# Kernel optimization log

Measured on AMD Instinct MI355X. Metric: run time of the kernel, lower is better.

The kernel has to match this reference:

```python
import jax, jax.numpy as jnp
import numpy as np

DIM = 1024
D_STATE = 16
D_CONV = 4
EXPAND = 2
D_INNER = EXPAND * DIM
BATCH = 4
SEQ = 2048


def setup_inputs() -> dict:
    key = jax.random.key(0)
    ks = jax.random.split(key, 9)
    n = lambda i, shape, scale=0.02: (jax.random.normal(ks[i], shape, jnp.float32) * scale)
    return {
        "x": jax.random.normal(ks[0], (BATCH, SEQ, DIM), jnp.float32),
        "in_proj_w": n(1, (D_INNER, DIM)),
        "conv_w": n(2, (D_INNER, D_CONV), 0.1),          # depthwise kernel (groups=d_inner)
        "x_proj_w": n(3, (2 * D_STATE + 1, D_INNER)),
        "dt_proj_w": n(4, (D_INNER, 1), 1.0),
        "dt_proj_b": n(5, (D_INNER,), 0.1),
        "A_log": jax.random.normal(ks[6], (D_INNER, D_STATE), jnp.float32),
        "D": jnp.ones((D_INNER,), jnp.float32),
        "out_proj_w": n(7, (DIM, D_INNER)),
        "norm_w": jnp.ones((DIM,), jnp.float32),
        "norm_b": jnp.zeros((DIM,), jnp.float32),
    }


def reference(x, in_proj_w, conv_w, x_proj_w, dt_proj_w, dt_proj_b,
              A_log, D, out_proj_w, norm_w, norm_b):
    Bsz, L, _ = x.shape
    shortcut = x

    # LayerNorm
    mu = jnp.mean(x, axis=-1, keepdims=True)
    var = jnp.var(x, axis=-1, keepdims=True)
    h = (x - mu) / jnp.sqrt(var + 1e-5) * norm_w + norm_b

    # in_proj: [B,L,dim] -> [B,L,d_inner]
    h = h @ in_proj_w.T

    # causal depthwise conv1d (padding d_conv-1, truncate to L)
    hp = jnp.pad(h, ((0, 0), (D_CONV - 1, 0), (0, 0)))
    h_conv = sum(hp[:, k:k + L, :] * conv_w[:, k] for k in range(D_CONV))
    h = jax.nn.silu(h_conv)

    # x_proj -> dt (1), B (d_state), C (d_state)
    proj = h @ x_proj_w.T
    dt_in = proj[..., :1]
    B_param = proj[..., 1:1 + D_STATE]      # [B,L,d_state]
    C_param = proj[..., 1 + D_STATE:]       # [B,L,d_state]
    dt = jax.nn.softplus(dt_in @ dt_proj_w.T + dt_proj_b)  # [B,L,d_inner]

    A = -jnp.exp(A_log)                     # [d_inner, d_state]

    def step(state, inp):
        dt_t, B_t, C_t, x_t = inp           # [B,d_inner],[B,ds],[B,ds],[B,d_inner]
        state = jnp.exp(A[None] * dt_t[:, :, None]) * state \
                + B_t[:, None, :] * x_t[:, :, None]          # [B,d_inner,d_state]
        y = jnp.einsum('bnd,bd->bn', state, C_t) + D * x_t   # [B,d_inner]
        return state, y

    init = jnp.zeros((Bsz, D_INNER, D_STATE), x.dtype)
    xs = (jnp.swapaxes(dt, 0, 1), jnp.swapaxes(B_param, 0, 1),
          jnp.swapaxes(C_param, 0, 1), jnp.swapaxes(h, 0, 1))
    state, ys = jax.lax.scan(step, init, xs)
    y = jnp.swapaxes(ys, 0, 1)              # [B,L,d_inner]

    out = jax.nn.silu(y) @ out_proj_w.T + shortcut
    return out, state
```

## Files before the change

### kernel.cpp

```cpp
#include <hip/hip_runtime.h>

typedef unsigned short u16;
typedef unsigned int u32;
typedef __attribute__((ext_vector_type(8))) short short8;
typedef __attribute__((ext_vector_type(4))) float f32x4;
typedef __attribute__((ext_vector_type(2))) float f32x2;
typedef __attribute__((ext_vector_type(8))) unsigned short ushort8_t;

#define SEQ 2048
#define DIM 1024
#define DINNER 2048
#define NPROJ 33
#define NPROJ_PAD 48
#define LC 32
#define NC 64

__device__ __forceinline__ u16 f2bf(float f) {
  union { float f; u32 u; } v; v.f = f;
  u32 r = (v.u + 0x7fffu + ((v.u >> 16) & 1u)) >> 16;
  return (u16)r;
}
__device__ __forceinline__ float bf2f(u16 s) {
  union { u32 u; float f; } v; v.u = ((u32)s) << 16;
  return v.f;
}
__device__ __forceinline__ float lo_bf(u32 w) {
  union { u32 u; float f; } v; v.u = w << 16; return v.f;
}
__device__ __forceinline__ float hi_bf(u32 w) {
  union { u32 u; float f; } v; v.u = w & 0xffff0000u; return v.f;
}
__device__ __forceinline__ float fexp2(float x) {
#if __has_builtin(__builtin_amdgcn_exp2f)
  return __builtin_amdgcn_exp2f(x);
#else
  return __expf(x * 0.69314718f);
#endif
}
__device__ __forceinline__ float softplus(float x) {
  return fmaxf(x, 0.f) + __logf(1.f + __expf(-fabsf(x)));
}
__device__ __forceinline__ f32x2 sp2(float v) { f32x2 r; r.x = v; r.y = v; return r; }
__device__ __forceinline__ f32x2 pkfma(f32x2 a, f32x2 b, f32x2 c) {
  return __builtin_elementwise_fma(a, b, c);
}
__device__ __forceinline__ void async16(const void* g, void* l) {
  __builtin_amdgcn_global_load_lds(
      (const __attribute__((address_space(1))) u32*)g,
      (__attribute__((address_space(3))) u32*)l, 16, 0, 0);
}

__global__ void cast_w_kernel(const float* __restrict__ w1, const float* __restrict__ w3,
                              u16* __restrict__ o1, u16* __restrict__ o3) {
  int i = blockIdx.x * 256 + threadIdx.x;
  float4 a = ((const float4*)w1)[i];
  float4 b = ((const float4*)w3)[i];
  ushort4 oa, ob;
  oa.x = f2bf(a.x); oa.y = f2bf(a.y); oa.z = f2bf(a.z); oa.w = f2bf(a.w);
  ob.x = f2bf(b.x); ob.y = f2bf(b.y); ob.z = f2bf(b.z); ob.w = f2bf(b.w);
  ((ushort4*)o1)[i] = oa;
  ((ushort4*)o3)[i] = ob;
}

__global__ void cast_w2pad_kernel(const float* __restrict__ src, u16* __restrict__ dst) {
  int i = blockIdx.x * 256 + threadIdx.x;
  int j = i >> 11, k = i & 2047;
  dst[i] = (j < NPROJ) ? f2bf(src[j * 2048 + k]) : (u16)0;
}

__global__ __launch_bounds__(256) void ln_kernel(const float* __restrict__ x,
                                                 const float* __restrict__ w,
                                                 const float* __restrict__ b,
                                                 u16* __restrict__ h) {
  const int row = blockIdx.x;
  const int tid = threadIdx.x;
  const int lane = tid & 63, wave = tid >> 6;
  const float4 v = ((const float4*)(x + (size_t)row * DIM))[tid];
  float s = v.x + v.y + v.z + v.w;
  float q = v.x * v.x + v.y * v.y + v.z * v.z + v.w * v.w;
  for (int off = 32; off; off >>= 1) {
    s += __shfl_down(s, off);
    q += __shfl_down(q, off);
  }
  __shared__ float sbuf[8];
  if (lane == 0) { sbuf[wave] = s; sbuf[4 + wave] = q; }
  __syncthreads();
  float tot = sbuf[0] + sbuf[1] + sbuf[2] + sbuf[3];
  float totq = sbuf[4] + sbuf[5] + sbuf[6] + sbuf[7];
  const float mean = tot * (1.0f / DIM);
  const float var = totq * (1.0f / DIM) - mean * mean;
  const float rs = rsqrtf(var + 1e-5f);
  const float4 wv = ((const float4*)w)[tid];
  const float4 bv = ((const float4*)b)[tid];
  ushort4 o;
  o.x = f2bf((v.x - mean) * rs * wv.x + bv.x);
  o.y = f2bf((v.y - mean) * rs * wv.y + bv.y);
  o.z = f2bf((v.z - mean) * rs * wv.z + bv.z);
  o.w = f2bf((v.w - mean) * rs * wv.w + bv.w);
  ((ushort4*)(h + (size_t)row * DIM))[tid] = o;
}

__global__ __launch_bounds__(512) void gemm_bf16_kernel(const u16* __restrict__ A,
                                                        const u16* __restrict__ Bt,
                                                        u16* __restrict__ C,
                                                        int K, int N) {
  __shared__ u16 As[128 * 32];
  __shared__ u16 Bs[128 * 32];
  const int tid = threadIdx.x;
  const int lane = tid & 63, wave = tid >> 6;
  const int wm = wave >> 2, wn = wave & 3;
  const int row16 = lane & 15, quad = lane >> 4;
  const int flat = blockIdx.x + gridDim.x * blockIdx.y;
  const int xcd = flat & 7;
  const int sidx = flat >> 3;
  const int bm = xcd * 8 + (sidx & 7);
  const int bn = sidx >> 3;
  f32x4 acc[4][2] = {};
  const u16* Ablk = A + (size_t)bm * 128 * K;
  const u16* Bblk = Bt + (size_t)bn * 128 * K;
  const int r = tid >> 2, cc = (tid & 3) * 8;
  for (int k0 = 0; k0 < K; k0 += 32) {
    async16(Ablk + (size_t)r * K + k0 + cc, &As[tid * 8]);
    async16(Bblk + (size_t)r * K + k0 + cc, &Bs[tid * 8]);
    __syncthreads();
    short8 af[4], bfr[2];
#pragma unroll
    for (int i = 0; i < 4; ++i)
      af[i] = *(const short8*)&As[(wm * 64 + i * 16 + row16) * 32 + quad * 8];
#pragma unroll
    for (int j = 0; j < 2; ++j)
      bfr[j] = *(const short8*)&Bs[(wn * 32 + j * 16 + row16) * 32 + quad * 8];
#pragma unroll
    for (int i = 0; i < 4; ++i)
#pragma unroll
      for (int j = 0; j < 2; ++j)
        acc[i][j] = __builtin_amdgcn_mfma_f32_16x16x32_bf16(af[i], bfr[j], acc[i][j], 0, 0, 0);
    __syncthreads();
  }
#pragma unroll
  for (int i = 0; i < 4; ++i) {
    int m = bm * 128 + wm * 64 + i * 16 + quad * 4;
#pragma unroll
    for (int j = 0; j < 2; ++j) {
      int n = bn * 128 + wn * 32 + j * 16 + row16;
#pragma unroll
      for (int rr = 0; rr < 4; ++rr)
        C[(size_t)(m + rr) * N + n] = f2bf(acc[i][j][rr]);
    }
  }
}

__global__ __launch_bounds__(512) void gemm_out_kernel(const u16* __restrict__ A,
                                                       const u16* __restrict__ Bt,
                                                       const float* __restrict__ resid,
                                                       float* __restrict__ C,
                                                       int K, int N) {
  __shared__ u16 As[128 * 32];
  __shared__ u16 Bs[128 * 32];
  const int tid = threadIdx.x;
  const int lane = tid & 63, wave = tid >> 6;
  const int wm = wave >> 2, wn = wave & 3;
  const int row16 = lane & 15, quad = lane >> 4;
  const int flat = blockIdx.x + gridDim.x * blockIdx.y;
  const int xcd = flat & 7;
  const int sidx = flat >> 3;
  const int bm = xcd * 8 + (sidx & 7);
  const int bn = sidx >> 3;
  f32x4 acc[4][2] = {};
  const u16* Ablk = A + (size_t)bm * 128 * K;
  const u16* Bblk = Bt + (size_t)bn * 128 * K;
  const int r = tid >> 2, cc = (tid & 3) * 8;
  for (int k0 = 0; k0 < K; k0 += 32) {
    async16(Ablk + (size_t)r * K + k0 + cc, &As[tid * 8]);
    async16(Bblk + (size_t)r * K + k0 + cc, &Bs[tid * 8]);
    __syncthreads();
    short8 af[4], bfr[2];
#pragma unroll
    for (int i = 0; i < 4; ++i)
      af[i] = *(const short8*)&As[(wm * 64 + i * 16 + row16) * 32 + quad * 8];
#pragma unroll
    for (int j = 0; j < 2; ++j)
      bfr[j] = *(const short8*)&Bs[(wn * 32 + j * 16 + row16) * 32 + quad * 8];
#pragma unroll
    for (int i = 0; i < 4; ++i)
#pragma unroll
      for (int j = 0; j < 2; ++j)
        acc[i][j] = __builtin_amdgcn_mfma_f32_16x16x32_bf16(af[i], bfr[j], acc[i][j], 0, 0, 0);
    __syncthreads();
  }
#pragma unroll
  for (int i = 0; i < 4; ++i) {
    int m = bm * 128 + wm * 64 + i * 16 + quad * 4;
#pragma unroll
    for (int j = 0; j < 2; ++j) {
      int n = bn * 128 + wn * 32 + j * 16 + row16;
#pragma unroll
      for (int rr = 0; rr < 4; ++rr) {
        size_t idx = (size_t)(m + rr) * N + n;
        C[idx] = acc[i][j][rr] + resid[idx];
      }
    }
  }
}

__global__ __launch_bounds__(256) void conv_silu_kernel(const u16* __restrict__ c1,
                                                        const float* __restrict__ cw,
                                                        u16* __restrict__ cs) {
  const int tid = threadIdx.x;
  const int dg = tid * 8;
  const size_t m0 = (size_t)blockIdx.x * 8;
  const int l0 = (int)(m0 & (SEQ - 1));
  float w[4][8];
  {
    const float4* cw4 = (const float4*)(cw + (size_t)dg * 4);
#pragma unroll
    for (int c = 0; c < 8; ++c) {
      float4 v = cw4[c];
      w[0][c] = v.x; w[1][c] = v.y; w[2][c] = v.z; w[3][c] = v.w;
    }
  }
  const u16* base = c1 + m0 * DINNER + dg;
  ushort8_t win0, win1, win2, win3;
  const ushort8_t zero = (ushort8_t)0;
  if (l0 == 0) {
    win0 = zero; win1 = zero; win2 = zero;
  } else {
    win0 = *(const ushort8_t*)(base - 3 * DINNER);
    win1 = *(const ushort8_t*)(base - 2 * DINNER);
    win2 = *(const ushort8_t*)(base - 1 * DINNER);
  }
  win3 = *(const ushort8_t*)(base);
#pragma unroll
  for (int t = 0; t < 8; ++t) {
    ushort8_t nxt = win3;
    if (t < 7) nxt = *(const ushort8_t*)(base + (size_t)(t + 1) * DINNER);
    ushort8_t o;
#pragma unroll
    for (int c = 0; c < 8; ++c) {
      float acc = bf2f((u16)win0[c]) * w[0][c];
      acc = fmaf(bf2f((u16)win1[c]), w[1][c], acc);
      acc = fmaf(bf2f((u16)win2[c]), w[2][c], acc);
      acc = fmaf(bf2f((u16)win3[c]), w[3][c], acc);
      const float s = acc / (1.f + __expf(-acc));
      o[c] = (unsigned short)f2bf(s);
    }
    *(ushort8_t*)(cs + (m0 + t) * DINNER + dg) = o;
    win0 = win1; win1 = win2; win2 = win3; win3 = nxt;
  }
}

__global__ __launch_bounds__(256) void gemm_w2_kernel(const u16* __restrict__ A,
                                                      const u16* __restrict__ Bt,
                                                      float* __restrict__ C) {
  __shared__ u16 As[64 * 32];
  __shared__ u16 Bs[48 * 32];
  const int tid = threadIdx.x;
  const int lane = tid & 63, wave = tid >> 6;
  const int row16 = lane & 15, quad = lane >> 4;
  const int bm = blockIdx.x;
  const int K = DINNER;
  f32x4 acc[3] = {};
  const u16* Ablk = A + (size_t)bm * 64 * K;
  const int r = tid >> 2, cc = (tid & 3) * 8;
  for (int k0 = 0; k0 < K; k0 += 32) {
    async16(Ablk + (size_t)r * K + k0 + cc, &As[tid * 8]);
    if (tid < 192) async16(Bt + (size_t)r * K + k0 + cc, &Bs[tid * 8]);
    __syncthreads();
    short8 af = *(const short8*)&As[(wave * 16 + row16) * 32 + quad * 8];
    short8 bfr[3];
#pragma unroll
    for (int j = 0; j < 3; ++j)
      bfr[j] = *(const short8*)&Bs[(j * 16 + row16) * 32 + quad * 8];
#pragma unroll
    for (int j = 0; j < 3; ++j)
      acc[j] = __builtin_amdgcn_mfma_f32_16x16x32_bf16(af, bfr[j], acc[j], 0, 0, 0);
    __syncthreads();
  }
  const int m = bm * 64 + wave * 16 + quad * 4;
#pragma unroll
  for (int j = 0; j < 3; ++j) {
    const int n = j * 16 + row16;
#pragma unroll
    for (int rr = 0; rr < 4; ++rr)
      C[(size_t)(m + rr) * NPROJ_PAD + n] = acc[j][rr];
  }
}


__global__ __launch_bounds__(128) void scan_phase1(const float* __restrict__ proj,
                                                   const u16* __restrict__ xs,
                                                   const float* __restrict__ dtw_,
                                                   const float* __restrict__ dtb_,
                                                   const float* __restrict__ A_log,
                                                   u16* __restrict__ S,
                                                   float* __restrict__ Tdt) {
  __shared__ float Bsh[LC][16];
  __shared__ float DTin[LC];
  const int tid = threadIdx.x;
  const int d0 = blockIdx.x * 256 + tid * 2;
  const int c = blockIdx.y;
  const int b = blockIdx.z;
  const size_t mrow = (size_t)b * SEQ + c * LC;
  for (int i = tid; i < LC * 16; i += 128) {
    int t = i >> 4, n = i & 15;
    Bsh[t][n] = proj[(mrow + t) * NPROJ_PAD + 1 + n];
  }
  if (tid < LC) DTin[tid] = proj[(mrow + tid) * NPROJ_PAD];
  __syncthreads();
  f32x2 An2[16];
#pragma unroll
  for (int n = 0; n < 16; ++n) {
    An2[n].x = -__expf(A_log[(size_t)d0 * 16 + n]) * 1.44269504f;
    An2[n].y = -__expf(A_log[(size_t)(d0 + 1) * 16 + n]) * 1.44269504f;
  }
  const float2 dtwv = *(const float2*)(dtw_ + d0);
  const float2 dtbv = *(const float2*)(dtb_ + d0);
  f32x2 dtw2; dtw2.x = dtwv.x; dtw2.y = dtwv.y;
  f32x2 dtb2; dtb2.x = dtbv.x; dtb2.y = dtbv.y;
  f32x2 s[16];
#pragma unroll
  for (int n = 0; n < 16; ++n) s[n] = sp2(0.f);
  f32x2 Tsum = sp2(0.f);
  const u16* xp = xs + mrow * DINNER + d0;
  u32 xw = *(const u32*)xp;
#pragma unroll 2
  for (int t = 0; t < LC; ++t) {
    f32x2 xv; xv.x = lo_bf(xw); xv.y = hi_bf(xw);
    if (t + 1 < LC) xw = *(const u32*)(xp + (size_t)(t + 1) * DINNER);
    f32x2 dtv = pkfma(sp2(DTin[t]), dtw2, dtb2);
    f32x2 sp; sp.x = softplus(dtv.x); sp.y = softplus(dtv.y);
    Tsum += sp;
    const float4* Br = (const float4*)&Bsh[t][0];
#pragma unroll
    for (int q = 0; q < 4; ++q) {
      const float4 Bq = Br[q];
      const float bqa[4] = {Bq.x, Bq.y, Bq.z, Bq.w};
#pragma unroll
      for (int j = 0; j < 4; ++j) {
        const int n = q * 4 + j;
        f32x2 e = An2[n] * sp;
        f32x2 dk; dk.x = fexp2(e.x); dk.y = fexp2(e.y);
        s[n] = pkfma(dk, s[n], sp2(bqa[j]) * xv);
      }
    }
  }
  const size_t so = ((size_t)(b * NC + c) * DINNER + d0) * 16;
  ushort8_t o0, o1, o2, o3;
#pragma unroll
  for (int j = 0; j < 8; ++j) {
    o0[j] = f2bf(s[j].x);     o1[j] = f2bf(s[8 + j].x);
    o2[j] = f2bf(s[j].y);     o3[j] = f2bf(s[8 + j].y);
  }
  *(ushort8_t*)(S + so) = o0;       *(ushort8_t*)(S + so + 8) = o1;
  *(ushort8_t*)(S + so + 16) = o2;  *(ushort8_t*)(S + so + 24) = o3;
  *(float2*)(Tdt + (size_t)(b * NC + c) * DINNER + d0) = make_float2(Tsum.x, Tsum.y);
}

__global__ __launch_bounds__(256) void scan_phase2(const float* __restrict__ A_log,
                                                   u16* __restrict__ S,
                                                   const float* __restrict__ Tdt,
                                                   float* __restrict__ out_state) {
  const int idx = blockIdx.x * 256 + threadIdx.x;
  const int nq = idx & 3;
  const int d = (idx >> 2) & (DINNER - 1);
  const int b = idx >> 13;
  float An2[4];
#pragma unroll
  for (int n = 0; n < 4; ++n) An2[n] = -__expf(A_log[d * 16 + nq * 4 + n]) * 1.44269504f;
  float prev[4] = {0.f, 0.f, 0.f, 0.f};
  for (int c = 0; c < NC; ++c) {
    const size_t base = (size_t)(b * NC + c) * DINNER + d;
    const float T = Tdt[base];
    const size_t so = base * 16 + nq * 4;
    ushort4 lv = *(const ushort4*)(S + so);
    const float loc[4] = {bf2f(lv.x), bf2f(lv.y), bf2f(lv.z), bf2f(lv.w)};
    ushort4 pv;
    pv.x = f2bf(prev[0]); pv.y = f2bf(prev[1]); pv.z = f2bf(prev[2]); pv.w = f2bf(prev[3]);
    *(ushort4*)(S + so) = pv;
    const float dk0 = fexp2(An2[0] * T), dk1 = fexp2(An2[1] * T);
    const float dk2 = fexp2(An2[2] * T), dk3 = fexp2(An2[3] * T);
    prev[0] = fmaf(dk0, prev[0], loc[0]);
    prev[1] = fmaf(dk1, prev[1], loc[1]);
    prev[2] = fmaf(dk2, prev[2], loc[2]);
    prev[3] = fmaf(dk3, prev[3], loc[3]);
  }
  *(float4*)(out_state + ((size_t)b * DINNER + d) * 16 + nq * 4) =
      make_float4(prev[0], prev[1], prev[2], prev[3]);
}

__global__ __launch_bounds__(128) void scan_phase3(const float* __restrict__ proj,
                                                   const u16* __restrict__ xs,
                                                   const float* __restrict__ dtw_,
                                                   const float* __restrict__ dtb_,
                                                   const float* __restrict__ A_log,
                                                   const float* __restrict__ Dp,
                                                   const u16* __restrict__ S,
                                                   u16* __restrict__ ysil) {
  __shared__ float Bsh[LC][16];
  __shared__ float Csh[LC][16];
  __shared__ float DTin[LC];
  const int tid = threadIdx.x;
  const int d0 = blockIdx.x * 256 + tid * 2;
  const int c = blockIdx.y;
  const int b = blockIdx.z;
  const size_t mrow = (size_t)b * SEQ + c * LC;
  for (int i = tid; i < LC * 16; i += 128) {
    int t = i >> 4, n = i & 15;
    Bsh[t][n] = proj[(mrow + t) * NPROJ_PAD + 1 + n];
    Csh[t][n] = proj[(mrow + t) * NPROJ_PAD + 17 + n];
  }
  if (tid < LC) DTin[tid] = proj[(mrow + tid) * NPROJ_PAD];
  __syncthreads();
  f32x2 An2[16];
#pragma unroll
  for (int n = 0; n < 16; ++n) {
    An2[n].x = -__expf(A_log[(size_t)d0 * 16 + n]) * 1.44269504f;
    An2[n].y = -__expf(A_log[(size_t)(d0 + 1) * 16 + n]) * 1.44269504f;
  }
  const float2 dtwv = *(const float2*)(dtw_ + d0);
  const float2 dtbv = *(const float2*)(dtb_ + d0);
  const float2 Ddv = *(const float2*)(Dp + d0);
  f32x2 dtw2; dtw2.x = dtwv.x; dtw2.y = dtwv.y;
  f32x2 dtb2; dtb2.x = dtbv.x; dtb2.y = dtbv.y;
  f32x2 Dd2; Dd2.x = Ddv.x; Dd2.y = Ddv.y;
  f32x2 s[16];
  const size_t so = ((size_t)(b * NC + c) * DINNER + d0) * 16;
  {
    ushort8_t v0 = *(const ushort8_t*)(S + so);
    ushort8_t v1 = *(const ushort8_t*)(S + so + 8);
    ushort8_t v2 = *(const ushort8_t*)(S + so + 16);
    ushort8_t v3 = *(const ushort8_t*)(S + so + 24);
#pragma unroll
    for (int j = 0; j < 8; ++j) {
      s[j].x = bf2f((u16)v0[j]);     s[8 + j].x = bf2f((u16)v1[j]);
      s[j].y = bf2f((u16)v2[j]);     s[8 + j].y = bf2f((u16)v3[j]);
    }
  }
  const u16* xp = xs + mrow * DINNER + d0;
  u16* yp = ysil + mrow * DINNER + d0;
  u32 xw = *(const u32*)xp;
#pragma unroll 2
  for (int t = 0; t < LC; ++t) {
    f32x2 xv; xv.x = lo_bf(xw); xv.y = hi_bf(xw);
    if (t + 1 < LC) xw = *(const u32*)(xp + (size_t)(t + 1) * DINNER);
    f32x2 dtv = pkfma(sp2(DTin[t]), dtw2, dtb2);
    f32x2 sp; sp.x = softplus(dtv.x); sp.y = softplus(dtv.y);
    f32x2 y = Dd2 * xv;
    const float4* Br = (const float4*)&Bsh[t][0];
    const float4* Cr = (const float4*)&Csh[t][0];
#pragma unroll
    for (int q = 0; q < 4; ++q) {
      const float4 Bq = Br[q];
      const float4 Cq = Cr[q];
      const float bqa[4] = {Bq.x, Bq.y, Bq.z, Bq.w};
      const float cqa[4] = {Cq.x, Cq.y, Cq.z, Cq.w};
#pragma unroll
      for (int j = 0; j < 4; ++j) {
        const int n = q * 4 + j;
        f32x2 e = An2[n] * sp;
        f32x2 dk; dk.x = fexp2(e.x); dk.y = fexp2(e.y);
        s[n] = pkfma(dk, s[n], sp2(bqa[j]) * xv);
        y = pkfma(sp2(cqa[j]), s[n], y);
      }
    }
    const float sy0 = y.x / (1.f + __expf(-y.x));
    const float sy1 = y.y / (1.f + __expf(-y.y));
    const u32 ow = (u32)f2bf(sy0) | ((u32)f2bf(sy1) << 16);
    *(u32*)(yp + (size_t)t * DINNER) = ow;
  }
}

extern "C" void kernel_launch(void* const* d_in, const int* in_sizes, int n_in,
                              void* d_out, int out_size, void* d_ws, size_t ws_size,
                              hipStream_t stream) {
  const float* x = (const float*)d_in[0];
  const float* in_proj_w = (const float*)d_in[1];
  const float* conv_w = (const float*)d_in[2];
  const float* x_proj_w = (const float*)d_in[3];
  const float* dt_proj_w = (const float*)d_in[4];
  const float* dt_proj_b = (const float*)d_in[5];
  const float* A_log = (const float*)d_in[6];
  const float* Dvec = (const float*)d_in[7];
  const float* out_proj_w = (const float*)d_in[8];
  const float* norm_w = (const float*)d_in[9];
  const float* norm_b = (const float*)d_in[10];

  char* ws = (char*)d_ws;
  u16* h = (u16*)(ws + 0);
  u16* w1b = (u16*)(ws + 16777216);
  u16* w3b = (u16*)(ws + 20971520);
  u16* w2b = (u16*)(ws + 25165824);
  u16* c1 = (u16*)(ws + 25362432);
  u16* ysil = c1;
  u16* cs = (u16*)(ws + 58916864);
  float* proj = (float*)(ws + 92471296);
  u16* Sbuf = (u16*)(ws + 94044160);
  float* Tdt = (float*)(ws + 110821376);

  float* out = (float*)d_out;
  float* out_state = out + (size_t)4 * SEQ * DIM;

  cast_w_kernel<<<2048, 256, 0, stream>>>(in_proj_w, out_proj_w, w1b, w3b);
  cast_w2pad_kernel<<<384, 256, 0, stream>>>(x_proj_w, w2b);
  ln_kernel<<<8192, 256, 0, stream>>>(x, norm_w, norm_b, h);
  gemm_bf16_kernel<<<dim3(DINNER / 128, 64), 512, 0, stream>>>(h, w1b, c1, DIM, DINNER);
  conv_silu_kernel<<<1024, 256, 0, stream>>>(c1, conv_w, cs);
  gemm_w2_kernel<<<128, 256, 0, stream>>>(cs, w2b, proj);
  scan_phase1<<<dim3(DINNER / 256, NC, 4), 128, 0, stream>>>(proj, cs, dt_proj_w, dt_proj_b,
                                                             A_log, Sbuf, Tdt);
  scan_phase2<<<128, 256, 0, stream>>>(A_log, Sbuf, Tdt, out_state);
  scan_phase3<<<dim3(DINNER / 256, NC, 4), 128, 0, stream>>>(proj, cs, dt_proj_w, dt_proj_b,
                                                             A_log, Dvec, Sbuf, ysil);
  gemm_out_kernel<<<dim3(DIM / 128, 64), 512, 0, stream>>>(ysil, w3b, x, out, DINNER, DIM);
}
```

Before: 379.0 us.

## Halve scan chunk length, widen phase2 parallelism, shrink w2 GEMM tiles, use fast reciprocal

Scan chunks shrink from 32 to 16 timesteps and the chunk count doubles, so phases 1 and 3 launch twice as many blocks. Phase 2 now gives each thread one state element instead of four, which quadruples its thread count. The x_proj GEMM uses 32-row tiles with 128 threads, and the SiLU divisions become hardware reciprocal multiplies. The chunk-state buffer now lives in the output buffer before the final GEMM overwrites it; the price is a longer sequential chunk chain and twice the chunk-state traffic.

```diff
diff --git a/kernel.cpp b/kernel.cpp
--- a/kernel.cpp
+++ b/kernel.cpp
@@ -12,8 +12,8 @@
 #define DINNER 2048
 #define NPROJ 33
 #define NPROJ_PAD 48
-#define LC 32
-#define NC 64
+#define LC 16
+#define NC 128
 
 __device__ __forceinline__ u16 f2bf(float f) {
   union { float f; u32 u; } v; v.f = f;
@@ -35,6 +35,13 @@
   return __builtin_amdgcn_exp2f(x);
 #else
   return __expf(x * 0.69314718f);
+#endif
+}
+__device__ __forceinline__ float frcp(float x) {
+#if __has_builtin(__builtin_amdgcn_rcpf)
+  return __builtin_amdgcn_rcpf(x);
+#else
+  return 1.f / x;
 #endif
 }
 __device__ __forceinline__ float softplus(float x) {
@@ -241,7 +248,7 @@
       acc = fmaf(bf2f((u16)win1[c]), w[1][c], acc);
       acc = fmaf(bf2f((u16)win2[c]), w[2][c], acc);
       acc = fmaf(bf2f((u16)win3[c]), w[3][c], acc);
-      const float s = acc / (1.f + __expf(-acc));
+      const float s = acc * frcp(1.f + __expf(-acc));
       o[c] = (unsigned short)f2bf(s);
     }
     *(ushort8_t*)(cs + (m0 + t) * DINNER + dg) = o;
@@ -249,10 +256,10 @@
   }
 }
 
-__global__ __launch_bounds__(256) void gemm_w2_kernel(const u16* __restrict__ A,
+__global__ __launch_bounds__(128) void gemm_w2_kernel(const u16* __restrict__ A,
                                                       const u16* __restrict__ Bt,
                                                       float* __restrict__ C) {
-  __shared__ u16 As[64 * 32];
+  __shared__ u16 As[32 * 32];
   __shared__ u16 Bs[48 * 32];
   const int tid = threadIdx.x;
   const int lane = tid & 63, wave = tid >> 6;
@@ -260,11 +267,13 @@
   const int bm = blockIdx.x;
   const int K = DINNER;
   f32x4 acc[3] = {};
-  const u16* Ablk = A + (size_t)bm * 64 * K;
+  const u16* Ablk = A + (size_t)bm * 32 * K;
   const int r = tid >> 2, cc = (tid & 3) * 8;
   for (int k0 = 0; k0 < K; k0 += 32) {
     async16(Ablk + (size_t)r * K + k0 + cc, &As[tid * 8]);
-    if (tid < 192) async16(Bt + (size_t)r * K + k0 + cc, &Bs[tid * 8]);
+    async16(Bt + (size_t)r * K + k0 + cc, &Bs[tid * 8]);
+    if (tid < 64)
+      async16(Bt + (size_t)(32 + r) * K + k0 + cc, &Bs[1024 + tid * 8]);
     __syncthreads();
     short8 af = *(const short8*)&As[(wave * 16 + row16) * 32 + quad * 8];
     short8 bfr[3];
@@ -276,7 +285,7 @@
       acc[j] = __builtin_amdgcn_mfma_f32_16x16x32_bf16(af, bfr[j], acc[j], 0, 0, 0);
     __syncthreads();
   }
-  const int m = bm * 64 + wave * 16 + quad * 4;
+  const int m = bm * 32 + wave * 16 + quad * 4;
 #pragma unroll
   for (int j = 0; j < 3; ++j) {
     const int n = j * 16 + row16;
@@ -361,31 +370,21 @@
                                                    const float* __restrict__ Tdt,
                                                    float* __restrict__ out_state) {
   const int idx = blockIdx.x * 256 + threadIdx.x;
-  const int nq = idx & 3;
-  const int d = (idx >> 2) & (DINNER - 1);
-  const int b = idx >> 13;
-  float An2[4];
-#pragma unroll
-  for (int n = 0; n < 4; ++n) An2[n] = -__expf(A_log[d * 16 + nq * 4 + n]) * 1.44269504f;
-  float prev[4] = {0.f, 0.f, 0.f, 0.f};
+  const int n = idx & 15;
+  const int d = (idx >> 4) & (DINNER - 1);
+  const int b = idx >> 15;
+  const float An = -__expf(A_log[d * 16 + n]) * 1.44269504f;
+  float prev = 0.f;
+#pragma unroll 4
   for (int c = 0; c < NC; ++c) {
     const size_t base = (size_t)(b * NC + c) * DINNER + d;
     const float T = Tdt[base];
-    const size_t so = base * 16 + nq * 4;
-    ushort4 lv = *(const ushort4*)(S + so);
-    const float loc[4] = {bf2f(lv.x), bf2f(lv.y), bf2f(lv.z), bf2f(lv.w)};
-    ushort4 pv;
-    pv.x = f2bf(prev[0]); pv.y = f2bf(prev[1]); pv.z = f2bf(prev[2]); pv.w = f2bf(prev[3]);
-    *(ushort4*)(S + so) = pv;
-    const float dk0 = fexp2(An2[0] * T), dk1 = fexp2(An2[1] * T);
-    const float dk2 = fexp2(An2[2] * T), dk3 = fexp2(An2[3] * T);
-    prev[0] = fmaf(dk0, prev[0], loc[0]);
-    prev[1] = fmaf(dk1, prev[1], loc[1]);
-    prev[2] = fmaf(dk2, prev[2], loc[2]);
-    prev[3] = fmaf(dk3, prev[3], loc[3]);
-  }
-  *(float4*)(out_state + ((size_t)b * DINNER + d) * 16 + nq * 4) =
-      make_float4(prev[0], prev[1], prev[2], prev[3]);
+    const size_t so = base * 16 + n;
+    const float loc = bf2f(S[so]);
+    S[so] = f2bf(prev);
+    prev = fmaf(fexp2(An * T), prev, loc);
+  }
+  out_state[((size_t)b * DINNER + d) * 16 + n] = prev;
 }
 
 __global__ __launch_bounds__(128) void scan_phase3(const float* __restrict__ proj,
@@ -463,8 +462,8 @@
         y = pkfma(sp2(cqa[j]), s[n], y);
       }
     }
-    const float sy0 = y.x / (1.f + __expf(-y.x));
-    const float sy1 = y.y / (1.f + __expf(-y.y));
+    const float sy0 = y.x * frcp(1.f + __expf(-y.x));
+    const float sy1 = y.y * frcp(1.f + __expf(-y.y));
     const u32 ow = (u32)f2bf(sy0) | ((u32)f2bf(sy1) << 16);
     *(u32*)(yp + (size_t)t * DINNER) = ow;
   }
@@ -494,21 +493,21 @@
   u16* ysil = c1;
   u16* cs = (u16*)(ws + 58916864);
   float* proj = (float*)(ws + 92471296);
-  u16* Sbuf = (u16*)(ws + 94044160);
-  float* Tdt = (float*)(ws + 110821376);
+  float* Tdt = (float*)(ws + 94044160);
 
   float* out = (float*)d_out;
   float* out_state = out + (size_t)4 * SEQ * DIM;
+  u16* Sbuf = (u16*)d_out;
 
   cast_w_kernel<<<2048, 256, 0, stream>>>(in_proj_w, out_proj_w, w1b, w3b);
   cast_w2pad_kernel<<<384, 256, 0, stream>>>(x_proj_w, w2b);
   ln_kernel<<<8192, 256, 0, stream>>>(x, norm_w, norm_b, h);
   gemm_bf16_kernel<<<dim3(DINNER / 128, 64), 512, 0, stream>>>(h, w1b, c1, DIM, DINNER);
   conv_silu_kernel<<<1024, 256, 0, stream>>>(c1, conv_w, cs);
-  gemm_w2_kernel<<<128, 256, 0, stream>>>(cs, w2b, proj);
+  gemm_w2_kernel<<<256, 128, 0, stream>>>(cs, w2b, proj);
   scan_phase1<<<dim3(DINNER / 256, NC, 4), 128, 0, stream>>>(proj, cs, dt_proj_w, dt_proj_b,
                                                              A_log, Sbuf, Tdt);
-  scan_phase2<<<128, 256, 0, stream>>>(A_log, Sbuf, Tdt, out_state);
+  scan_phase2<<<512, 256, 0, stream>>>(A_log, Sbuf, Tdt, out_state);
   scan_phase3<<<dim3(DINNER / 256, NC, 4), 128, 0, stream>>>(proj, cs, dt_proj_w, dt_proj_b,
                                                              A_log, Dvec, Sbuf, ysil);
   gemm_out_kernel<<<dim3(DIM / 128, 64), 512, 0, stream>>>(ysil, w3b, x, out, DINNER, DIM);
```

After: 366.7 us. -3.2%, faster.
